# Kernel optimization log

Hardware: AMD Instinct MI355X
Metric: run time of the kernel (lower is better)

Reference implementation:

```python
import jax, jax.numpy as jnp
import numpy as np

N = 100000      # nodes
E = 1600000     # edges (avg degree 16)
IN = 512        # input feature dim
H, C = 8, 8     # conv1: 8 heads x 8 channels (hardcoded in module)
HID = H * C     # 64
OUT = 64        # output classes (conv2: 1 head, no concat)
NEG_SLOPE = 0.2 # PyG GATConv default leaky-relu slope


def setup_inputs() -> dict:
    key = jax.random.key(0)
    ks = jax.random.split(key, 10)
    x = jax.random.normal(ks[0], (N, IN), dtype=jnp.float32)
    edge_index = jax.random.randint(ks[1], (2, E), 0, N, dtype=jnp.int32)
    W1 = jax.random.normal(ks[2], (IN, HID), dtype=jnp.float32) / np.sqrt(IN).astype(np.float32)
    a_src1 = jax.random.normal(ks[3], (H, C), dtype=jnp.float32) * 0.1
    a_dst1 = jax.random.normal(ks[4], (H, C), dtype=jnp.float32) * 0.1
    b1 = jnp.zeros((HID,), dtype=jnp.float32)
    W2 = jax.random.normal(ks[5], (HID, OUT), dtype=jnp.float32) / np.sqrt(HID).astype(np.float32)
    a_src2 = jax.random.normal(ks[6], (1, OUT), dtype=jnp.float32) * 0.1
    a_dst2 = jax.random.normal(ks[7], (1, OUT), dtype=jnp.float32) * 0.1
    b2 = jnp.zeros((OUT,), dtype=jnp.float32)
    return {"x": x, "edge_index": edge_index, "W1": W1, "a_src1": a_src1,
            "a_dst1": a_dst1, "b1": b1, "W2": W2, "a_src2": a_src2,
            "a_dst2": a_dst2, "b2": b2}


def _gat_attend(h, src, dst, a_s, a_d, n_nodes):
    """h: [N,H,C]; src/dst: [E]; a_s/a_d: [H,C] -> aggregated [N,H,C]."""
    # per-node half-scores (PyG decomposition of a^T [Wx_i || Wx_j])
    sc_s = jnp.sum(h * a_s, axis=-1)                       # [N,H]
    sc_d = jnp.sum(h * a_d, axis=-1)                       # [N,H]
    logits = jax.nn.leaky_relu(sc_s[src] + sc_d[dst], NEG_SLOPE)  # [E,H]
    # segment softmax over edges grouped by destination node
    mx = jax.ops.segment_max(logits, dst, num_segments=n_nodes)   # [N,H]
    ex = jnp.exp(logits - mx[dst])                          # [E,H]
    denom = jax.ops.segment_sum(ex, dst, num_segments=n_nodes)    # [N,H]
    alpha = ex / (denom[dst] + 1e-16)                       # [E,H]
    msg = h[src] * alpha[:, :, None]                        # [E,H,C]
    return jax.ops.segment_sum(msg, dst, num_segments=n_nodes)    # [N,H,C]


def reference(x, edge_index, W1, a_src1, a_dst1, b1, W2, a_src2, a_dst2, b2):
    n = x.shape[0]
    loop = jnp.arange(n, dtype=edge_index.dtype)
    src = jnp.concatenate([edge_index[0], loop])            # self-loops (PyG default)
    dst = jnp.concatenate([edge_index[1], loop])
    # conv1: 8 heads, concat
    h1 = (x @ W1).reshape(n, H, C)
    o1 = _gat_attend(h1, src, dst, a_src1, a_dst1, n).reshape(n, HID) + b1
    x2 = jax.nn.elu(o1)
    # conv2: 1 head, no concat
    h2 = (x2 @ W2).reshape(n, 1, OUT)
    o2 = _gat_attend(h2, src, dst, a_src2, a_dst2, n)[:, 0] + b2
    return jax.nn.log_softmax(o2, axis=1)
```

## Files before the change

### kernel.cpp

```cpp
#include <hip/hip_runtime.h>
#include <cstdint>
#include <cstddef>

#define LEAKY 0.2f
#define NEG_INF -3.402823466e38f
static const int CHUNK = 2048;

typedef __attribute__((ext_vector_type(8))) short short8;
typedef __attribute__((ext_vector_type(4))) float floatx4;

__device__ __forceinline__ unsigned short f2bf(float f) {
    unsigned u = __float_as_uint(f);
    u += 0x7fffu + ((u >> 16) & 1u);
    return (unsigned short)(u >> 16);
}
__device__ __forceinline__ float bf2f(unsigned short u) {
    return __uint_as_float(((unsigned)u) << 16);
}
__device__ __forceinline__ float bflo(unsigned u) { return __uint_as_float(u << 16); }
__device__ __forceinline__ float bfhi(unsigned u) { return __uint_as_float(u & 0xffff0000u); }

__global__ __launch_bounds__(256) void k_misc(const float* __restrict__ W1, unsigned short* __restrict__ W1t,
                                              int* __restrict__ deg8, int Nn) {
    int i = blockIdx.x * 256 + threadIdx.x;
    if (i < 64 * 512) {
        int n = i >> 9, k = i & 511;
        W1t[i] = f2bf(W1[k * 64 + n]);
    }
    if (i < 8 * Nn) deg8[i] = 0;
}

__global__ __launch_bounds__(256) void k_mega1(const float* __restrict__ A, const unsigned short* __restrict__ W1t,
                                               unsigned short* __restrict__ C,
                                               const float* __restrict__ as1, const float* __restrict__ ad1,
                                               float* __restrict__ scs, float* __restrict__ scd, int M,
                                               const int* __restrict__ ei, int* __restrict__ deg8, int E, int G1) {
    __shared__ __align__(16) unsigned short As[2][128][40];
    __shared__ __align__(16) unsigned short Bs[2][64][40];

    if ((int)blockIdx.x >= G1) {
        int cb = blockIdx.x - G1;
        int nthr = 1024 * 256;
        int tid = cb * 256 + threadIdx.x;
        int* mydeg = deg8 + (size_t)(cb & 7) * M;
        for (int e = tid; e < E; e += nthr) {
            int d = ei[E + e];
            atomicAdd(&mydeg[d], 1);
        }
        return;
    }

    int t = threadIdx.x;
    int w = t >> 6, l = t & 63;
    int quad = l >> 4, lm = l & 15;
    int row0 = blockIdx.x * 128;

    const float* aptr[4];
#pragma unroll
    for (int j = 0; j < 4; ++j) {
        int f = t + 256 * j;
        int r = f >> 3, c4 = f & 7;
        int rg = row0 + r; if (rg >= M) rg = M - 1;
        aptr[j] = A + (size_t)rg * 512 + c4 * 4;
    }
    int bn = t >> 2, bseg = t & 3;
    const unsigned short* bptr = W1t + (size_t)bn * 512 + bseg * 8;
    int sr = t >> 3, sc4 = t & 7;

    floatx4 acc[2][4] = {};
    float4 va[4];
    uint4 vb;

#pragma unroll
    for (int j = 0; j < 4; ++j) va[j] = *(const float4*)(aptr[j] + 0);
    vb = *(const uint4*)(bptr + 0);
#pragma unroll
    for (int j = 0; j < 4; ++j) {
        ushort4 b; b.x = f2bf(va[j].x); b.y = f2bf(va[j].y); b.z = f2bf(va[j].z); b.w = f2bf(va[j].w);
        *(ushort4*)&As[0][sr + 32 * j][sc4 * 4] = b;
    }
    *(uint4*)&Bs[0][bn][bseg * 8] = vb;
    __syncthreads();

#pragma unroll
    for (int kt = 0; kt < 16; ++kt) {
        int cur = kt & 1;
        if (kt < 15) {
            int k0 = (kt + 1) * 32;
#pragma unroll
            for (int j = 0; j < 4; ++j) va[j] = *(const float4*)(aptr[j] + k0);
            vb = *(const uint4*)(bptr + k0);
        }

        short8 af[2], bfm[4];
#pragma unroll
        for (int tm = 0; tm < 2; ++tm) {
            int m = w * 32 + tm * 16 + lm;
            af[tm] = *(const short8*)&As[cur][m][quad * 8];
        }
#pragma unroll
        for (int tn = 0; tn < 4; ++tn) {
            int n = tn * 16 + lm;
            bfm[tn] = *(const short8*)&Bs[cur][n][quad * 8];
        }
#pragma unroll
        for (int tm = 0; tm < 2; ++tm)
#pragma unroll
            for (int tn = 0; tn < 4; ++tn)
                acc[tm][tn] = __builtin_amdgcn_mfma_f32_16x16x32_bf16(af[tm], bfm[tn], acc[tm][tn], 0, 0, 0);

        if (kt < 15) {
            int nxt = cur ^ 1;
#pragma unroll
            for (int j = 0; j < 4; ++j) {
                ushort4 b; b.x = f2bf(va[j].x); b.y = f2bf(va[j].y); b.z = f2bf(va[j].z); b.w = f2bf(va[j].w);
                *(ushort4*)&As[nxt][sr + 32 * j][sc4 * 4] = b;
            }
            *(uint4*)&Bs[nxt][bn][bseg * 8] = vb;
        }
        __syncthreads();
    }

    float as_l[4], ad_l[4];
#pragma unroll
    for (int tn = 0; tn < 4; ++tn) { as_l[tn] = as1[tn * 16 + lm]; ad_l[tn] = ad1[tn * 16 + lm]; }
    int hbase = (l >> 3) & 1;

#pragma unroll
    for (int tm = 0; tm < 2; ++tm) {
#pragma unroll
        for (int r = 0; r < 4; ++r) {
            int row = row0 + w * 32 + tm * 16 + quad * 4 + r;
            if (row < M) {
#pragma unroll
                for (int tn = 0; tn < 4; ++tn)
                    C[(size_t)row * 64 + tn * 16 + lm] = f2bf(acc[tm][tn][r]);
                float ps[4], pd[4];
#pragma unroll
                for (int tn = 0; tn < 4; ++tn) {
                    ps[tn] = acc[tm][tn][r] * as_l[tn];
                    pd[tn] = acc[tm][tn][r] * ad_l[tn];
                }
#pragma unroll
                for (int o = 1; o < 8; o <<= 1) {
#pragma unroll
                    for (int tn = 0; tn < 4; ++tn) {
                        ps[tn] += __shfl_xor(ps[tn], o);
                        pd[tn] += __shfl_xor(pd[tn], o);
                    }
                }
                if ((l & 7) == 0) {
#pragma unroll
                    for (int tn = 0; tn < 4; ++tn) {
                        scs[(size_t)row * 8 + tn * 2 + hbase] = ps[tn];
                        scd[(size_t)row * 8 + tn * 2 + hbase] = pd[tn];
                    }
                }
            }
        }
    }
}

__global__ __launch_bounds__(256) void k_scan1(const int* __restrict__ deg8, int* __restrict__ deg,
                                               int* __restrict__ bsum, int Nn) {
    __shared__ int sm[256];
    int b = blockIdx.x, t = threadIdx.x;
    int s = 0;
    int i0 = b * CHUNK + t * 8;
#pragma unroll
    for (int j = 0; j < 8; ++j) {
        int i = i0 + j;
        if (i < Nn) {
            int d = 1;
#pragma unroll
            for (int p = 0; p < 8; ++p) d += deg8[(size_t)p * Nn + i];
            deg[i] = d;
            s += d;
        }
    }
    sm[t] = s;
    __syncthreads();
    for (int o = 128; o; o >>= 1) { if (t < o) sm[t] += sm[t + o]; __syncthreads(); }
    if (t == 0) bsum[b] = sm[0];
}

__global__ __launch_bounds__(256) void k_scan3(const int* __restrict__ deg, const int* __restrict__ bsum,
                                               int* __restrict__ indptr, int* __restrict__ cursor,
                                               int Nn, int B) {
    __shared__ int wsum[4];
    int b = blockIdx.x, t = threadIdx.x, lane = t & 63, w = t >> 6;

    int vb = (lane < B) ? bsum[lane] : 0;
    int incb = vb;
#pragma unroll
    for (int o = 1; o < 64; o <<= 1) { int u = __shfl_up(incb, o); if (lane >= o) incb += u; }
    int bpre_b = __shfl(incb - vb, b);

    int i0 = b * CHUNK + t * 8;
    int d[8]; int s = 0;
#pragma unroll
    for (int j = 0; j < 8; ++j) { int i = i0 + j; d[j] = (i < Nn) ? deg[i] : 0; s += d[j]; }
    int inc = s;
#pragma unroll
    for (int o = 1; o < 64; o <<= 1) { int u = __shfl_up(inc, o); if (lane >= o) inc += u; }
    if (lane == 63) wsum[w] = inc;
    __syncthreads();
    int wofs = 0;
    for (int k = 0; k < w; ++k) wofs += wsum[k];
    int base = bpre_b + wofs + (inc - s);
    int run = 0;
#pragma unroll
    for (int j = 0; j < 8; ++j) {
        int i = i0 + j;
        if (i < Nn) {
            int v = base + run;
            indptr[i] = v; cursor[i] = v;
            run += d[j];
            if (i == Nn - 1) indptr[Nn] = v + d[j];
        }
    }
}

__global__ __launch_bounds__(256) void k_fill_p(const int* __restrict__ ei, int* __restrict__ cursor,
                                                int* __restrict__ csr, int E, int Nn) {
    int part = blockIdx.x & 7;
    int lo = (int)((long long)Nn * part >> 3);
    int hi = (int)((long long)Nn * (part + 1) >> 3);
    int nthr = (gridDim.x >> 3) * 256;
    int tid = (blockIdx.x >> 3) * 256 + threadIdx.x;
    int tot = E + Nn;
    for (int idx = tid; idx < tot; idx += nthr) {
        int d = (idx < E) ? ei[E + idx] : idx - E;
        if (d >= lo && d < hi) {
            int s = (idx < E) ? ei[idx] : idx - E;
            int slot = atomicAdd(&cursor[d], 1);
            csr[slot] = s;
        }
    }
}

template <int KB>
__global__ __launch_bounds__(256) void gemm_n64(const float* __restrict__ A, const float* __restrict__ B,
                                                unsigned short* __restrict__ C,
                                                const float* __restrict__ as2, const float* __restrict__ ad2,
                                                float* __restrict__ sc2s, float* __restrict__ sc2d,
                                                int M, int K) {
    __shared__ float As[KB][68];
    __shared__ float Bs[KB][68];
    int tid = threadIdx.x;
    int row0 = blockIdx.x * 64;
    int tx = tid & 15, ty = tid >> 4;
    float acc[4][4] = {};
    for (int k0 = 0; k0 < K; k0 += KB) {
#pragma unroll
        for (int j = 0; j < (64 * KB) / (256 * 4); ++j) {
            int f = tid + 256 * j;
            int r = f / (KB / 4);
            int c4 = f % (KB / 4);
            int rg = row0 + r; if (rg >= M) rg = M - 1;
            float4 v = *(const float4*)(A + (size_t)rg * K + k0 + c4 * 4);
            As[c4 * 4 + 0][r] = v.x; As[c4 * 4 + 1][r] = v.y;
            As[c4 * 4 + 2][r] = v.z; As[c4 * 4 + 3][r] = v.w;
        }
#pragma unroll
        for (int j = 0; j < (KB * 64) / (256 * 4); ++j) {
            int f = tid + 256 * j;
            int kk = f / 16, c4 = f % 16;
            *(float4*)&Bs[kk][c4 * 4] = *(const float4*)(B + (size_t)(k0 + kk) * 64 + c4 * 4);
        }
        __syncthreads();
#pragma unroll
        for (int kk = 0; kk < KB; ++kk) {
            float4 a = *(const float4*)&As[kk][ty * 4];
            float4 b = *(const float4*)&Bs[kk][tx * 4];
            float av[4] = {a.x, a.y, a.z, a.w};
            float bv[4] = {b.x, b.y, b.z, b.w};
#pragma unroll
            for (int i = 0; i < 4; ++i)
#pragma unroll
                for (int j = 0; j < 4; ++j) acc[i][j] += av[i] * bv[j];
        }
        __syncthreads();
    }
    float as_l[4], ad_l[4];
#pragma unroll
    for (int j = 0; j < 4; ++j) { as_l[j] = as2[tx * 4 + j]; ad_l[j] = ad2[tx * 4 + j]; }
#pragma unroll
    for (int i = 0; i < 4; ++i) {
        int rg = row0 + ty * 4 + i;
        if (rg < M) {
            ushort4 b; b.x = f2bf(acc[i][0]); b.y = f2bf(acc[i][1]);
            b.z = f2bf(acc[i][2]); b.w = f2bf(acc[i][3]);
            *(ushort4*)(C + (size_t)rg * 64 + tx * 4) = b;
            float ps = acc[i][0] * as_l[0] + acc[i][1] * as_l[1] + acc[i][2] * as_l[2] + acc[i][3] * as_l[3];
            float pd = acc[i][0] * ad_l[0] + acc[i][1] * ad_l[1] + acc[i][2] * ad_l[2] + acc[i][3] * ad_l[3];
#pragma unroll
            for (int o = 1; o < 16; o <<= 1) { ps += __shfl_xor(ps, o); pd += __shfl_xor(pd, o); }
            if (tx == 0) { sc2s[rg] = ps; sc2d[rg] = pd; }
        }
    }
}

__global__ __launch_bounds__(256) void k_agg1(const unsigned short* __restrict__ h1, const float* __restrict__ scs,
                                              const float* __restrict__ scd, const int* __restrict__ indptr,
                                              const int* __restrict__ csr, const float* __restrict__ b1,
                                              float* __restrict__ x2, int Nn) {
    int node = (blockIdx.x * 256 + threadIdx.x) >> 6;
    int l = threadIdx.x & 63;
    if (node >= Nn) return;
    int h8 = l & 7, grp = l >> 3;
    int start = indptr[node], end = indptr[node + 1];
    float sd = scd[node * 8 + h8];

    float dsum = 0.f;
    float acc8[8] = {};
    for (int base = start; base < end; base += 64) {
        int e = base + l;
        int s64 = csr[e < end ? e : start];
        int cnt = min(64, end - base);
        int nb = (cnt + 7) >> 3;
#pragma unroll
        for (int b = 0; b < 8; ++b) {
            if (b < nb) {
                int slot = base + b * 8 + grp;
                int sb = __shfl(s64, b * 8 + grp);
                float v = scs[sb * 8 + h8] + sd;
                v = v > 0.f ? v : LEAKY * v;
                float ex = (slot < end) ? __expf(v) : 0.f;
                dsum += ex;
                uint4 q = *(const uint4*)(h1 + (size_t)sb * 64 + h8 * 8);
                acc8[0] += ex * bflo(q.x); acc8[1] += ex * bfhi(q.x);
                acc8[2] += ex * bflo(q.y); acc8[3] += ex * bfhi(q.y);
                acc8[4] += ex * bflo(q.z); acc8[5] += ex * bfhi(q.z);
                acc8[6] += ex * bflo(q.w); acc8[7] += ex * bfhi(q.w);
            }
        }
    }
#pragma unroll
    for (int o = 8; o < 64; o <<= 1) {
        dsum += __shfl_xor(dsum, o);
#pragma unroll
        for (int k = 0; k < 8; ++k) acc8[k] += __shfl_xor(acc8[k], o);
    }
    if (grp == 0) {
        float inv = 1.f / (dsum + 1e-16f);
        float4 ba = *((const float4*)b1 + h8 * 2);
        float4 bb = *((const float4*)b1 + h8 * 2 + 1);
        float o0 = acc8[0] * inv + ba.x, o1 = acc8[1] * inv + ba.y;
        float o2 = acc8[2] * inv + ba.z, o3 = acc8[3] * inv + ba.w;
        float o4 = acc8[4] * inv + bb.x, o5 = acc8[5] * inv + bb.y;
        float o6 = acc8[6] * inv + bb.z, o7 = acc8[7] * inv + bb.w;
        o0 = o0 > 0.f ? o0 : expm1f(o0); o1 = o1 > 0.f ? o1 : expm1f(o1);
        o2 = o2 > 0.f ? o2 : expm1f(o2); o3 = o3 > 0.f ? o3 : expm1f(o3);
        o4 = o4 > 0.f ? o4 : expm1f(o4); o5 = o5 > 0.f ? o5 : expm1f(o5);
        o6 = o6 > 0.f ? o6 : expm1f(o6); o7 = o7 > 0.f ? o7 : expm1f(o7);
        float* dst = x2 + (size_t)node * 64 + h8 * 8;
        *(float4*)dst = make_float4(o0, o1, o2, o3);
        *(float4*)(dst + 4) = make_float4(o4, o5, o6, o7);
    }
}

__global__ __launch_bounds__(256) void k_agg2(const unsigned short* __restrict__ h2, const float* __restrict__ scs,
                                              const float* __restrict__ scd, const int* __restrict__ indptr,
                                              const int* __restrict__ csr, const float* __restrict__ b2,
                                              float* __restrict__ out, int Nn) {
    int node = (blockIdx.x * 256 + threadIdx.x) >> 6;
    int l = threadIdx.x & 63;
    if (node >= Nn) return;
    int g = l >> 3, c8 = l & 7;
    int start = indptr[node], end = indptr[node + 1];
    float sd = scd[node];

    float dsum = 0.f;
    float acc8[8] = {};
    for (int base = start; base < end; base += 64) {
        int e = base + l;
        int s64 = csr[e < end ? e : start];
        float v = scs[s64] + sd;
        v = v > 0.f ? v : LEAKY * v;
        float ex = (e < end) ? __expf(v) : 0.f;
        dsum += ex;
        int cnt = min(64, end - base);
        int nb = (cnt + 7) >> 3;
#pragma unroll 2
        for (int b = 0; b < nb; ++b) {
            float exv = __shfl(ex, b * 8 + g);
            int sb = __shfl(s64, b * 8 + g);
            uint4 q = *(const uint4*)(h2 + (size_t)sb * 64 + c8 * 8);
            acc8[0] += exv * bflo(q.x); acc8[1] += exv * bfhi(q.x);
            acc8[2] += exv * bflo(q.y); acc8[3] += exv * bfhi(q.y);
            acc8[4] += exv * bflo(q.z); acc8[5] += exv * bfhi(q.z);
            acc8[6] += exv * bflo(q.w); acc8[7] += exv * bfhi(q.w);
        }
    }
#pragma unroll
    for (int o = 32; o; o >>= 1) dsum += __shfl_xor(dsum, o);
#pragma unroll
    for (int o = 8; o < 64; o <<= 1)
#pragma unroll
        for (int k = 0; k < 8; ++k) acc8[k] += __shfl_xor(acc8[k], o);

    float inv = 1.f / (dsum + 1e-16f);
    float4 ba = *((const float4*)b2 + c8 * 2);
    float4 bb = *((const float4*)b2 + c8 * 2 + 1);
    float ov[8];
    ov[0] = acc8[0] * inv + ba.x; ov[1] = acc8[1] * inv + ba.y;
    ov[2] = acc8[2] * inv + ba.z; ov[3] = acc8[3] * inv + ba.w;
    ov[4] = acc8[4] * inv + bb.x; ov[5] = acc8[5] * inv + bb.y;
    ov[6] = acc8[6] * inv + bb.z; ov[7] = acc8[7] * inv + bb.w;

    float m2 = ov[0];
#pragma unroll
    for (int k = 1; k < 8; ++k) m2 = fmaxf(m2, ov[k]);
#pragma unroll
    for (int o = 1; o < 8; o <<= 1) m2 = fmaxf(m2, __shfl_xor(m2, o));
    float se = 0.f;
#pragma unroll
    for (int k = 0; k < 8; ++k) se += __expf(ov[k] - m2);
#pragma unroll
    for (int o = 1; o < 8; o <<= 1) se += __shfl_xor(se, o);
    float ls = m2 + __logf(se);
    if (g == 0) {
        float* dst = out + (size_t)node * 64 + c8 * 8;
        *(float4*)dst = make_float4(ov[0] - ls, ov[1] - ls, ov[2] - ls, ov[3] - ls);
        *(float4*)(dst + 4) = make_float4(ov[4] - ls, ov[5] - ls, ov[6] - ls, ov[7] - ls);
    }
}

extern "C" void kernel_launch(void* const* d_in, const int* in_sizes, int n_in,
                              void* d_out, int out_size, void* d_ws, size_t ws_size,
                              hipStream_t stream) {
    (void)n_in; (void)out_size; (void)ws_size;
    const float* x   = (const float*)d_in[0];
    const int*   ei  = (const int*)d_in[1];
    const float* W1  = (const float*)d_in[2];
    const float* as1 = (const float*)d_in[3];
    const float* ad1 = (const float*)d_in[4];
    const float* b1  = (const float*)d_in[5];
    const float* W2  = (const float*)d_in[6];
    const float* as2 = (const float*)d_in[7];
    const float* ad2 = (const float*)d_in[8];
    const float* b2  = (const float*)d_in[9];
    float* out = (float*)d_out;

    const int N = in_sizes[0] / 512;
    const int E = in_sizes[1] / 2;

    char* p = (char*)d_ws;
    auto alloc = [&](size_t bytes) -> char* {
        char* r = p; p += (bytes + 255) & ~(size_t)255; return r;
    };
    unsigned short* h1bf = (unsigned short*)alloc((size_t)N * 64 * 2);
    float* x2    = (float*)alloc((size_t)N * 64 * 4);
    unsigned short* h2bf = h1bf;
    float* sc1s  = (float*)alloc((size_t)N * 8 * 4);
    float* sc1d  = (float*)alloc((size_t)N * 8 * 4);
    float* sc2s  = (float*)alloc((size_t)N * 4);
    float* sc2d  = (float*)alloc((size_t)N * 4);
    int*   deg   = (int*)alloc((size_t)N * 4);
    int*   deg8  = (int*)alloc((size_t)N * 8 * 4);
    int*   cursor= (int*)alloc((size_t)N * 4);
    int*   indptr= (int*)alloc((size_t)(N + 1) * 4);
    int*   csr   = (int*)alloc((size_t)(E + N) * 4);
    int*   bsum  = (int*)alloc(64 * 4);
    unsigned short* W1t = (unsigned short*)alloc(64 * 512 * 2);

    const int B = (N + CHUNK - 1) / CHUNK;
    const int G1 = (N + 127) / 128;

    const long long miscElems = (64 * 512 > 8 * (long long)N) ? 64 * 512 : 8 * (long long)N;
    k_misc<<<(int)((miscElems + 255) / 256), 256, 0, stream>>>(W1, W1t, deg8, N);

    k_mega1<<<G1 + 1024, 256, 0, stream>>>(x, W1t, h1bf, as1, ad1, sc1s, sc1d, N,
                                           ei, deg8, E, G1);

    k_scan1 <<<B, 256, 0, stream>>>(deg8, deg, bsum, N);
    k_scan3 <<<B, 256, 0, stream>>>(deg, bsum, indptr, cursor, N, B);
    k_fill_p<<<1024, 256, 0, stream>>>(ei, cursor, csr, E, N);

    k_agg1<<<(N + 3) / 4, 256, 0, stream>>>(h1bf, sc1s, sc1d, indptr, csr, b1, x2, N);

    gemm_n64<64><<<(N + 63) / 64, 256, 0, stream>>>(x2, W2, h2bf, as2, ad2, sc2s, sc2d, N, 64);

    k_agg2<<<(N + 3) / 4, 256, 0, stream>>>(h2bf, sc2s, sc2d, indptr, csr, b2, out, N);
}
```

Measured before the change: 558.8 us.

## Use per-partition privatized cursors for CSR fill and write self-loops in scan

CSR construction now gives each of the 8 degree-histogram partitions its own cursor array, with sub-offsets computed during the scan. Each fill block takes one partition via blockIdx&7 and reads edges only once. This replaces the old scheme where each of 8 passes scanned all edges and filtered by destination range. Self-loop entries are written directly by the scan kernel. It relies on the edge-to-partition assignment in k_mega1 matching blockIdx&7 and 1024 fill blocks; a mismatch would overflow slots. The order of neighbours within each row becomes nondeterministic.

```diff
diff --git a/kernel.cpp b/kernel.cpp
--- a/kernel.cpp
+++ b/kernel.cpp
@@ -184,9 +184,10 @@
     if (t == 0) bsum[b] = sm[0];
 }
 
-__global__ __launch_bounds__(256) void k_scan3(const int* __restrict__ deg, const int* __restrict__ bsum,
-                                               int* __restrict__ indptr, int* __restrict__ cursor,
-                                               int Nn, int B) {
+__global__ __launch_bounds__(256) void k_scan3(const int* __restrict__ deg, const int* __restrict__ deg8,
+                                               const int* __restrict__ bsum,
+                                               int* __restrict__ indptr, int* __restrict__ cursor8,
+                                               int* __restrict__ csr, int Nn, int B) {
     __shared__ int wsum[4];
     int b = blockIdx.x, t = threadIdx.x, lane = t & 63, w = t >> 6;
 
@@ -214,28 +215,31 @@
         int i = i0 + j;
         if (i < Nn) {
             int v = base + run;
-            indptr[i] = v; cursor[i] = v;
+            indptr[i] = v;
+            csr[v] = i;
+            int cb2 = v + 1;
+#pragma unroll
+            for (int p = 0; p < 8; ++p) {
+                cursor8[(size_t)p * Nn + i] = cb2;
+                cb2 += deg8[(size_t)p * Nn + i];
+            }
             run += d[j];
             if (i == Nn - 1) indptr[Nn] = v + d[j];
         }
     }
 }
 
-__global__ __launch_bounds__(256) void k_fill_p(const int* __restrict__ ei, int* __restrict__ cursor,
-                                                int* __restrict__ csr, int E, int Nn) {
-    int part = blockIdx.x & 7;
-    int lo = (int)((long long)Nn * part >> 3);
-    int hi = (int)((long long)Nn * (part + 1) >> 3);
-    int nthr = (gridDim.x >> 3) * 256;
-    int tid = (blockIdx.x >> 3) * 256 + threadIdx.x;
-    int tot = E + Nn;
-    for (int idx = tid; idx < tot; idx += nthr) {
-        int d = (idx < E) ? ei[E + idx] : idx - E;
-        if (d >= lo && d < hi) {
-            int s = (idx < E) ? ei[idx] : idx - E;
-            int slot = atomicAdd(&cursor[d], 1);
-            csr[slot] = s;
-        }
+__global__ __launch_bounds__(256) void k_fill_priv(const int* __restrict__ ei, int* __restrict__ cursor8,
+                                                   int* __restrict__ csr, int E, int Nn) {
+    int cb = blockIdx.x;
+    int nthr = 1024 * 256;
+    int tid = cb * 256 + threadIdx.x;
+    int* mycur = cursor8 + (size_t)(cb & 7) * Nn;
+    for (int e = tid; e < E; e += nthr) {
+        int d = ei[E + e];
+        int s = ei[e];
+        int slot = atomicAdd(&mycur[d], 1);
+        csr[slot] = s;
     }
 }
 
@@ -459,7 +463,7 @@
     float* sc2d  = (float*)alloc((size_t)N * 4);
     int*   deg   = (int*)alloc((size_t)N * 4);
     int*   deg8  = (int*)alloc((size_t)N * 8 * 4);
-    int*   cursor= (int*)alloc((size_t)N * 4);
+    int*   cursor8 = (int*)alloc((size_t)N * 8 * 4);
     int*   indptr= (int*)alloc((size_t)(N + 1) * 4);
     int*   csr   = (int*)alloc((size_t)(E + N) * 4);
     int*   bsum  = (int*)alloc(64 * 4);
@@ -474,9 +478,9 @@
     k_mega1<<<G1 + 1024, 256, 0, stream>>>(x, W1t, h1bf, as1, ad1, sc1s, sc1d, N,
                                            ei, deg8, E, G1);
 
-    k_scan1 <<<B, 256, 0, stream>>>(deg8, deg, bsum, N);
-    k_scan3 <<<B, 256, 0, stream>>>(deg, bsum, indptr, cursor, N, B);
-    k_fill_p<<<1024, 256, 0, stream>>>(ei, cursor, csr, E, N);
+    k_scan1   <<<B, 256, 0, stream>>>(deg8, deg, bsum, N);
+    k_scan3   <<<B, 256, 0, stream>>>(deg, deg8, bsum, indptr, cursor8, csr, N, B);
+    k_fill_priv<<<1024, 256, 0, stream>>>(ei, cursor8, csr, E, N);
 
     k_agg1<<<(N + 3) / 4, 256, 0, stream>>>(h1bf, sc1s, sc1d, indptr, csr, b1, x2, N);
 
```

After: 583.4 us. 4.4% more time.
